# Optimization experiments

Hardware: AMD Instinct MI355X
Metric: run time of the kernel (lower is better)

Reference implementation:

```python
import jax, jax.numpy as jnp
import numpy as np


def setup_inputs() -> dict:
    key = jax.random.key(0)
    ks = jax.random.split(key, 8)
    B, S, H = 2, 2048, 2048
    Hq, Hkv, D = 16, 4, H // 16
    s = 0.02
    return {
        "query": jax.random.normal(ks[0], (B, S, H), jnp.float32),
        "key": jax.random.normal(ks[1], (B, S, H), jnp.float32),
        "value": jax.random.normal(ks[2], (B, S, H), jnp.float32),
        "Wq": jax.random.normal(ks[3], (H, Hq * D), jnp.float32) * s,
        "bq": jnp.zeros((Hq * D,), jnp.float32),
        "Wk": jax.random.normal(ks[4], (H, Hkv * D), jnp.float32) * s,
        "bk": jnp.zeros((Hkv * D,), jnp.float32),
        "Wv": jax.random.normal(ks[5], (H, Hkv * D), jnp.float32) * s,
        "bv": jnp.zeros((Hkv * D,), jnp.float32),
        "Wo": jax.random.normal(ks[6], (H, H), jnp.float32) * s,
        "bo": jnp.zeros((H,), jnp.float32),
    }


def reference(query, key, value, Wq, bq, Wk, bk, Wv, bv, Wo, bo):
    Hq, Hkv = 16, 4
    B, S, H = query.shape
    D = H // Hq
    G = Hq // Hkv  # heads per KV group
    # projections
    q = query @ Wq + bq   # [B,S,Hq*D]
    k = key @ Wk + bk     # [B,S,Hkv*D]
    v = value @ Wv + bv   # [B,S,Hkv*D]
    # [B, Hkv(groups), G(heads per group), S, D] for q; [B, Hkv, S, D] for k,v
    q = q.reshape(B, S, Hkv, G, D).transpose(0, 2, 3, 1, 4)
    k = k.reshape(B, S, Hkv, D).transpose(0, 2, 1, 3)
    v = v.reshape(B, S, Hkv, D).transpose(0, 2, 1, 3)
    # NOTE: original module applies NO 1/sqrt(D) scaling -- kept faithful.
    attn = jnp.einsum('bghqd,bgkd->bghqk', q, k)  # [B,Hkv,G,S,S]
    attn = jax.nn.softmax(attn, axis=-1)
    out = jnp.einsum('bghqk,bgkd->bghqd', attn, v)  # [B,Hkv,G,S,D]
    # permute(0,3,1,2,4) -> [B,S,Hkv,G,D] -> [B,S,H]
    out = out.transpose(0, 3, 1, 2, 4).reshape(B, S, H)
    return out @ Wo + bo
```

## Files before the change

### kernel.cpp

```cpp
#include <hip/hip_runtime.h>
#include <hip/hip_bf16.h>
#include <type_traits>
#include <stdint.h>

typedef short bf16x8 __attribute__((ext_vector_type(8)));
typedef float f32x4 __attribute__((ext_vector_type(4)));

#define GLL16(gp, lp) __builtin_amdgcn_global_load_lds( \
    (const __attribute__((address_space(1))) void*)(gp), \
    (__attribute__((address_space(3))) void*)(lp), 16, 0, 0)

__device__ inline short f2bf(float f) {
    union { float f; uint32_t u; } v;
    v.f = f;
    uint32_t r = (v.u + 0x7FFFu + ((v.u >> 16) & 1u)) >> 16;
    return (short)(uint16_t)r;
}

__device__ inline bf16x8 cvt8(const float4& a, const float4& b) {
    bf16x8 o;
    o[0] = f2bf(a.x); o[1] = f2bf(a.y); o[2] = f2bf(a.z); o[3] = f2bf(a.w);
    o[4] = f2bf(b.x); o[5] = f2bf(b.y); o[6] = f2bf(b.z); o[7] = f2bf(b.w);
    return o;
}

__global__ __launch_bounds__(256) void cvtk(const float* __restrict__ in,
                                            short* __restrict__ out, int n8)
{
    int i = blockIdx.x * blockDim.x + threadIdx.x;
    int stride = gridDim.x * blockDim.x;
    for (; i < n8; i += stride) {
        const float4* p = (const float4*)(in + (size_t)i * 8);
        float4 a = p[0], b = p[1];
        *(bf16x8*)(out + (size_t)i * 8) = cvt8(a, b);
    }
}

__global__ __launch_bounds__(256) void cvt3(
    const float* __restrict__ q, const float* __restrict__ k, const float* __restrict__ v,
    short* __restrict__ Xq, short* __restrict__ Xk, short* __restrict__ Xv)
{
    const float* in; short* out;
    if (blockIdx.y == 0) { in = q; out = Xq; }
    else if (blockIdx.y == 1) { in = k; out = Xk; }
    else { in = v; out = Xv; }
    size_t i = (size_t)blockIdx.x * 256 + threadIdx.x;
    const float4* p = (const float4*)(in + i * 8);
    float4 a = p[0], b = p[1];
    *(bf16x8*)(out + i * 8) = cvt8(a, b);
}

__global__ __launch_bounds__(256) void transW4(
    const float* __restrict__ W0, const float* __restrict__ W1,
    const float* __restrict__ W2, const float* __restrict__ W3,
    short* __restrict__ T0, short* __restrict__ T1,
    short* __restrict__ T2, short* __restrict__ T3)
{
    const int K = 2048;
    const float* W; short* T; int N;
    int z = blockIdx.z;
    if (z == 0)      { W = W0; T = T0; N = 2048; }
    else if (z == 1) { W = W1; T = T1; N = 512; }
    else if (z == 2) { W = W2; T = T2; N = 512; }
    else             { W = W3; T = T3; N = 2048; }
    int n0 = blockIdx.x * 64, k0 = blockIdx.y * 64;
    if (n0 >= N) return;
    __shared__ short Tt[64][65];
    int t = threadIdx.x;
    int kl = t >> 2, nb = (t & 3) * 16;
    const float* wp = W + (size_t)(k0 + kl) * N + n0 + nb;
    #pragma unroll
    for (int j = 0; j < 16; ++j) Tt[nb + j][kl] = f2bf(wp[j]);
    __syncthreads();
    int nl = t >> 2, kb = (t & 3) * 16;
    short* op = T + (size_t)(n0 + nl) * K + k0 + kb;
    #pragma unroll
    for (int j = 0; j < 16; ++j) op[j] = Tt[nl][kb + j];
}

__global__ __launch_bounds__(256) void transV(const short* __restrict__ Vb,
                                              short* __restrict__ Vt)
{
    __shared__ short T[64][65];
    int s0 = blockIdx.x * 64, d0 = blockIdx.y * 64, bg = blockIdx.z;
    int b = bg >> 2, g = bg & 3;
    int t = threadIdx.x;
    int sl = t >> 2, db = (t & 3) * 16;
    const short* vp = Vb + (size_t)(b * 2048 + s0 + sl) * 512 + g * 128 + d0 + db;
    #pragma unroll
    for (int j = 0; j < 16; ++j) T[db + j][sl] = vp[j];
    __syncthreads();
    int dl = t >> 2, sb = (t & 3) * 16;
    short* op = Vt + (size_t)(bg * 128 + d0 + dl) * 2048 + s0 + sb;
    #pragma unroll
    for (int j = 0; j < 16; ++j) op[j] = T[dl][sb + j];
}

template <typename TC>
__device__ __forceinline__ void gemm_core(
    const short* __restrict__ A, const short* __restrict__ BT,
    const float* __restrict__ bias, TC* __restrict__ C,
    int N, int K, int m0, int n0, short* As, short* Bs)
{
    const int t = threadIdx.x, w = t >> 6, lane = t & 63;
    const int lr = lane & 15, lg = lane >> 4;
    const int wm = (w >> 1) * 64, wn = (w & 1) * 64;
    f32x4 acc[4][4] = {};

    const int lrow = lane >> 3;
    const int lcg = (lane & 7) ^ (lrow & 7);
    const int sw = lr & 7;

    const short* abase[2]; const short* bbase[2];
    #pragma unroll
    for (int kc = 0; kc < 2; ++kc) {
        abase[kc] = &As[(wm + lr) * 64 + (((kc * 4 + lg) ^ sw) * 8)];
        bbase[kc] = &Bs[(wn + lr) * 64 + (((kc * 4 + lg) ^ sw) * 8)];
    }
    const short* asrc = A  + (size_t)(m0 + w * 32 + lrow) * K + lcg * 8;
    const short* bsrc = BT + (size_t)(n0 + w * 32 + lrow) * K + lcg * 8;
    short* adst = &As[(w * 32) * 64];
    short* bdst = &Bs[(w * 32) * 64];

    for (int kk = 0; kk < K; kk += 64) {
        __syncthreads();
        #pragma unroll
        for (int i = 0; i < 4; ++i) {
            GLL16(asrc + (size_t)i * 8 * K, adst + i * 512);
            GLL16(bsrc + (size_t)i * 8 * K, bdst + i * 512);
        }
        asrc += 64; bsrc += 64;
        __syncthreads();
        #pragma unroll
        for (int kc = 0; kc < 2; ++kc) {
            bf16x8 af[4], bfr[4];
            #pragma unroll
            for (int i = 0; i < 4; ++i) af[i] = *(const bf16x8*)(abase[kc] + i * 1024);
            #pragma unroll
            for (int j = 0; j < 4; ++j) bfr[j] = *(const bf16x8*)(bbase[kc] + j * 1024);
            #pragma unroll
            for (int i = 0; i < 4; ++i)
                #pragma unroll
                for (int j = 0; j < 4; ++j)
                    acc[i][j] = __builtin_amdgcn_mfma_f32_16x16x32_bf16(af[i], bfr[j], acc[i][j], 0, 0, 0);
        }
    }

    #pragma unroll
    for (int i = 0; i < 4; ++i) {
        #pragma unroll
        for (int j = 0; j < 4; ++j) {
            #pragma unroll
            for (int r = 0; r < 4; ++r) {
                int row = m0 + wm + i * 16 + lg * 4 + r;
                int col = n0 + wn + j * 16 + lr;
                float v = acc[i][j][r] + bias[col];
                if constexpr (std::is_same<TC, short>::value)
                    C[(size_t)row * N + col] = f2bf(v);
                else
                    C[(size_t)row * N + col] = v;
            }
        }
    }
}

template <typename TC>
__global__ __launch_bounds__(256) void gemm_std(
    const short* __restrict__ A, const short* __restrict__ BT,
    const float* __restrict__ bias, TC* __restrict__ C, int N, int K)
{
    __shared__ short As[128 * 64];
    __shared__ short Bs[128 * 64];
    int bid = blockIdx.x;
    int chunk = gridDim.x >> 3;
    int wg = (bid & 7) * chunk + (bid >> 3);
    int m0 = (wg & 31) * 128, n0 = (wg >> 5) * 128;
    gemm_core<TC>(A, BT, bias, C, N, K, m0, n0, As, Bs);
}

__global__ __launch_bounds__(256) void gemm_qkv(
    const short* __restrict__ Xq, const short* __restrict__ Xk, const short* __restrict__ Xv,
    const short* __restrict__ WqT, const short* __restrict__ WkT, const short* __restrict__ WvT,
    const float* __restrict__ bq, const float* __restrict__ bk, const float* __restrict__ bv,
    short* __restrict__ Qb, short* __restrict__ Kb, short* __restrict__ Vb)
{
    __shared__ short As[128 * 64];
    __shared__ short Bs[128 * 64];
    int bid = blockIdx.x;
    int wg = (bid & 7) * 96 + (bid >> 3);
    const short* A; const short* BT; const float* bi; short* C; int N; int l;
    if (wg < 512)      { l = wg;      A = Xq; BT = WqT; bi = bq; C = Qb; N = 2048; }
    else if (wg < 640) { l = wg - 512; A = Xk; BT = WkT; bi = bk; C = Kb; N = 512; }
    else               { l = wg - 640; A = Xv; BT = WvT; bi = bv; C = Vb; N = 512; }
    int m0 = (l & 31) * 128, n0 = (l >> 5) * 128;
    gemm_core<short>(A, BT, bi, C, N, 2048, m0, n0, As, Bs);
}

__global__ __launch_bounds__(256, 4) void attn_kernel(
    const short* __restrict__ Qb, const short* __restrict__ Kb,
    const short* __restrict__ Vt, short* __restrict__ Ob)
{
    const int S = 2048;
    __shared__ short Ks[64 * 128];
    __shared__ short Vs[128 * 64];
    __shared__ short Pl[4][8 * 128];

    const int qt = blockIdx.x, bh = blockIdx.y;
    const int b = bh >> 4, h = bh & 15, g = h >> 2, bg = b * 4 + g;
    const int t = threadIdx.x, w = t >> 6, lane = t & 63;
    const int lr = lane & 15, lg = lane >> 4;
    const int q0 = qt * 64 + w * 16;
    const float C = 1.44269504089f;

    const short* qrow = Qb + ((size_t)(b * S + q0 + lr) * 2048) + h * 128;
    bf16x8 qf[4];
    #pragma unroll
    for (int kc = 0; kc < 4; ++kc)
        qf[kc] = *(const bf16x8*)(qrow + kc * 32 + lg * 8);

    f32x4 ao[8] = {};
    float m_r[4], l_r[4];
    #pragma unroll
    for (int r = 0; r < 4; ++r) { m_r[r] = -1e30f; l_r[r] = 0.0f; }

    const int sw = lr & 7;
    const short* kbase[4];
    #pragma unroll
    for (int kc = 0; kc < 4; ++kc)
        kbase[kc] = &Ks[lr * 128 + (((kc * 4 + lg) ^ sw) * 8)];
    const short* vbase[2];
    #pragma unroll
    for (int kc = 0; kc < 2; ++kc)
        vbase[kc] = &Vs[lr * 64 + (((kc * 4 + lg) ^ sw) * 8)];
    short* Pw = &Pl[w][0];
    short* pwb = Pw + ((lr >> 3) * 128 + lg * 32 + (lr & 7));
    const short* prb = Pw + (lg * 128 + lr * 8);

    const int Lr4 = lane >> 4, Lc4 = lane & 15;
    const int Lr3 = lane >> 3, Lc3 = lane & 7;
    const short* ksrc[4]; const short* vsrc[4];
    #pragma unroll
    for (int i = 0; i < 4; ++i) {
        int kr = w * 16 + i * 4 + Lr4;
        ksrc[i] = Kb + (size_t)(b * S + kr) * 512 + g * 128 + (Lc4 ^ (kr & 7)) * 8;
        int vr = w * 32 + i * 8 + Lr3;
        vsrc[i] = Vt + (size_t)(bg * 128 + vr) * 2048 + (Lc3 ^ (vr & 7)) * 8;
    }
    short* kdst = &Ks[(w * 16) * 128];
    short* vdst = &Vs[(w * 32) * 64];

    for (int kv0 = 0; kv0 < S; kv0 += 64) {
        __syncthreads();
        #pragma unroll
        for (int i = 0; i < 4; ++i) {
            GLL16(ksrc[i], kdst + i * 512);
            GLL16(vsrc[i], vdst + i * 512);
        }
        #pragma unroll
        for (int i = 0; i < 4; ++i) { ksrc[i] += 64 * 512; vsrc[i] += 64; }
        __syncthreads();

        f32x4 sc[4] = {};
        #pragma unroll
        for (int kc = 0; kc < 4; ++kc) {
            #pragma unroll
            for (int f = 0; f < 4; ++f) {
                bf16x8 kfr = *(const bf16x8*)(kbase[kc] + f * 2048);
                sc[f] = __builtin_amdgcn_mfma_f32_16x16x32_bf16(qf[kc], kfr, sc[f], 0, 0, 0);
            }
        }

        float mx[4];
        #pragma unroll
        for (int r = 0; r < 4; ++r) {
            float m = fmaxf(fmaxf(sc[0][r], sc[1][r]), fmaxf(sc[2][r], sc[3][r]));
            m = fmaxf(m, __shfl_xor(m, 1));
            m = fmaxf(m, __shfl_xor(m, 2));
            m = fmaxf(m, __shfl_xor(m, 4));
            m = fmaxf(m, __shfl_xor(m, 8));
            mx[r] = m;
        }
        bool need = (mx[0] > m_r[0]) | (mx[1] > m_r[1]) | (mx[2] > m_r[2]) | (mx[3] > m_r[3]);
        if (__any(need)) {
            float sf[4];
            #pragma unroll
            for (int r = 0; r < 4; ++r) {
                float mnew = fmaxf(m_r[r], mx[r]);
                sf[r] = exp2f((m_r[r] - mnew) * C);
                m_r[r] = mnew;
                l_r[r] *= sf[r];
            }
            #pragma unroll
            for (int d0 = 0; d0 < 8; ++d0)
                #pragma unroll
                for (int r = 0; r < 4; ++r)
                    ao[d0][r] *= sf[r];
        }
        #pragma unroll
        for (int r = 0; r < 4; ++r) {
            float nmc = -m_r[r] * C;
            float p0 = exp2f(fmaf(sc[0][r], C, nmc));
            float p1 = exp2f(fmaf(sc[1][r], C, nmc));
            float p2 = exp2f(fmaf(sc[2][r], C, nmc));
            float p3 = exp2f(fmaf(sc[3][r], C, nmc));
            float rs = (p0 + p1) + (p2 + p3);
            rs += __shfl_xor(rs, 1);
            rs += __shfl_xor(rs, 2);
            rs += __shfl_xor(rs, 4);
            rs += __shfl_xor(rs, 8);
            l_r[r] += rs;
            pwb[0 * 256 + r * 8] = f2bf(p0);
            pwb[1 * 256 + r * 8] = f2bf(p1);
            pwb[2 * 256 + r * 8] = f2bf(p2);
            pwb[3 * 256 + r * 8] = f2bf(p3);
        }

        bf16x8 pf0 = *(const bf16x8*)(prb);
        bf16x8 pf1 = *(const bf16x8*)(prb + 512);
        #pragma unroll
        for (int d0 = 0; d0 < 8; ++d0) {
            bf16x8 v0 = *(const bf16x8*)(vbase[0] + d0 * 1024);
            bf16x8 v1 = *(const bf16x8*)(vbase[1] + d0 * 1024);
            ao[d0] = __builtin_amdgcn_mfma_f32_16x16x32_bf16(pf0, v0, ao[d0], 0, 0, 0);
            ao[d0] = __builtin_amdgcn_mfma_f32_16x16x32_bf16(pf1, v1, ao[d0], 0, 0, 0);
        }
    }

    #pragma unroll
    for (int d0 = 0; d0 < 8; ++d0) {
        #pragma unroll
        for (int r = 0; r < 4; ++r) {
            float v = ao[d0][r] / l_r[r];
            int q = q0 + lg * 4 + r;
            Ob[(size_t)(b * S + q) * 2048 + h * 128 + d0 * 16 + lr] = f2bf(v);
        }
    }
}

extern "C" void kernel_launch(void* const* d_in, const int* in_sizes, int n_in,
                              void* d_out, int out_size, void* d_ws, size_t ws_size,
                              hipStream_t stream)
{
    const float* query = (const float*)d_in[0];
    const float* key   = (const float*)d_in[1];
    const float* value = (const float*)d_in[2];
    const float* Wq    = (const float*)d_in[3];
    const float* bq    = (const float*)d_in[4];
    const float* Wk    = (const float*)d_in[5];
    const float* bk    = (const float*)d_in[6];
    const float* Wv    = (const float*)d_in[7];
    const float* bv    = (const float*)d_in[8];
    const float* Wo    = (const float*)d_in[9];
    const float* bo    = (const float*)d_in[10];
    float* out = (float*)d_out;

    const int BS = 4096;
    char* ws = (char*)d_ws;
    dim3 blk(256);

    if (ws_size >= (size_t)100663296) {
        short* Xq  = (short*)(ws + 0);
        short* Xk  = (short*)(ws + 16777216);
        short* Xv  = (short*)(ws + 33554432);
        short* Qb  = (short*)(ws + 50331648);
        short* Kb  = (short*)(ws + 67108864);
        short* Vb  = (short*)(ws + 71303168);
        short* Vtg = (short*)(ws + 75497472);
        short* WqT = (short*)(ws + 79691776);
        short* WkT = (short*)(ws + 88080384);
        short* WvT = (short*)(ws + 90177536);
        short* WoT = (short*)(ws + 92274688);
        short* Ob  = Xq;

        transW4<<<dim3(32, 32, 4), blk, 0, stream>>>(Wq, Wk, Wv, Wo, WqT, WkT, WvT, WoT);
        cvt3<<<dim3(4096, 3), blk, 0, stream>>>(query, key, value, Xq, Xk, Xv);
        gemm_qkv<<<768, blk, 0, stream>>>(Xq, Xk, Xv, WqT, WkT, WvT, bq, bk, bv, Qb, Kb, Vb);
        transV<<<dim3(32, 2, 8), blk, 0, stream>>>(Vb, Vtg);
        attn_kernel<<<dim3(32, 32), blk, 0, stream>>>(Qb, Kb, Vtg, Ob);
        gemm_std<float><<<512, blk, 0, stream>>>(Ob, WoT, bo, out, 2048, 2048);
    } else {
        short* Qb  = (short*)(ws + 0);
        short* Kb  = (short*)(ws + 16777216);
        short* Vb  = (short*)(ws + 20971520);
        short* Vtg = (short*)(ws + 25165824);
        short* WqT = (short*)(ws + 29360128);
        short* WkT = (short*)(ws + 37748736);
        short* WvT = (short*)(ws + 39845888);
        short* WoT = (short*)(ws + 41943040);
        short* Xbf = (short*)(ws + 50331648);

        transW4<<<dim3(32, 32, 4), blk, 0, stream>>>(Wq, Wk, Wv, Wo, WqT, WkT, WvT, WoT);
        cvtk<<<2048, blk, 0, stream>>>(query, Xbf, BS * 2048 / 8);
        gemm_std<short><<<512, blk, 0, stream>>>(Xbf, WqT, bq, Qb, 2048, 2048);
        cvtk<<<2048, blk, 0, stream>>>(key, Xbf, BS * 2048 / 8);
        gemm_std<short><<<128, blk, 0, stream>>>(Xbf, WkT, bk, Kb, 512, 2048);
        cvtk<<<2048, blk, 0, stream>>>(value, Xbf, BS * 2048 / 8);
        gemm_std<short><<<128, blk, 0, stream>>>(Xbf, WvT, bv, Vb, 512, 2048);
        transV<<<dim3(32, 2, 8), blk, 0, stream>>>(Vb, Vtg);
        attn_kernel<<<dim3(32, 32), blk, 0, stream>>>(Qb, Kb, Vtg, Xbf);
        gemm_std<float><<<512, blk, 0, stream>>>(Xbf, WoT, bo, out, 2048, 2048);
    }
}
```

Baseline: 313.8 us.

## Rewrite attention with 32x32 MFMA, transposed scores, register P and double-buffered K/V

The attention kernel moves from 16x16x32 to 32x32x16 MFMA tiles and computes S^T so each lane owns one query row. Softmax then needs only one cross-half shuffle. P is packed to bf16 in registers and exchanged with lane shuffles instead of going through LDS, K/V tiles are double-buffered so the next tile loads while the current one computes, and block IDs are remapped for locality. Each block now covers 128 query rows and occupancy is halved (launch bounds 2), trading more registers per thread for fewer LDS round-trips and more MFMA reuse of K/V.

```diff
diff --git a/kernel.cpp b/kernel.cpp
--- a/kernel.cpp
+++ b/kernel.cpp
@@ -4,7 +4,9 @@
 #include <stdint.h>
 
 typedef short bf16x8 __attribute__((ext_vector_type(8)));
+typedef short short4v __attribute__((ext_vector_type(4)));
 typedef float f32x4 __attribute__((ext_vector_type(4)));
+typedef float f32x16 __attribute__((ext_vector_type(16)));
 
 #define GLL16(gp, lp) __builtin_amdgcn_global_load_lds( \
     (const __attribute__((address_space(1))) void*)(gp), \
@@ -22,6 +24,31 @@
     o[0] = f2bf(a.x); o[1] = f2bf(a.y); o[2] = f2bf(a.z); o[3] = f2bf(a.w);
     o[4] = f2bf(b.x); o[5] = f2bf(b.y); o[6] = f2bf(b.z); o[7] = f2bf(b.w);
     return o;
+}
+
+__device__ inline uint32_t cvtpk(float lo, float hi) {
+    uint32_t r;
+    asm("v_cvt_pk_bf16_f32 %0, %1, %2" : "=v"(r) : "v"(lo), "v"(hi));
+    return r;
+}
+
+__device__ inline bf16x8 mk8(uint32_t a, uint32_t b, uint32_t c, uint32_t d) {
+    union { uint32_t u[4]; bf16x8 v; } t;
+    t.u[0] = a; t.u[1] = b; t.u[2] = c; t.u[3] = d;
+    return t.v;
+}
+
+__device__ inline void xchg_pf(const uint32_t c[8], bool hib, bf16x8& fA, bf16x8& fB) {
+    uint32_t p0 = (uint32_t)__shfl_xor((int)c[0], 32);
+    uint32_t p1 = (uint32_t)__shfl_xor((int)c[1], 32);
+    uint32_t p2 = (uint32_t)__shfl_xor((int)c[2], 32);
+    uint32_t p3 = (uint32_t)__shfl_xor((int)c[3], 32);
+    fA = mk8(hib ? p2 : c[0], hib ? p3 : c[1], hib ? c[2] : p0, hib ? c[3] : p1);
+    uint32_t p4 = (uint32_t)__shfl_xor((int)c[4], 32);
+    uint32_t p5 = (uint32_t)__shfl_xor((int)c[5], 32);
+    uint32_t p6 = (uint32_t)__shfl_xor((int)c[6], 32);
+    uint32_t p7 = (uint32_t)__shfl_xor((int)c[7], 32);
+    fB = mk8(hib ? p6 : c[4], hib ? p7 : c[5], hib ? c[6] : p4, hib ? c[7] : p5);
 }
 
 __global__ __launch_bounds__(256) void cvtk(const float* __restrict__ in,
@@ -189,150 +216,148 @@
     int bid = blockIdx.x;
     int wg = (bid & 7) * 96 + (bid >> 3);
     const short* A; const short* BT; const float* bi; short* C; int N; int l;
-    if (wg < 512)      { l = wg;      A = Xq; BT = WqT; bi = bq; C = Qb; N = 2048; }
+    if (wg < 512)      { l = wg;       A = Xq; BT = WqT; bi = bq; C = Qb; N = 2048; }
     else if (wg < 640) { l = wg - 512; A = Xk; BT = WkT; bi = bk; C = Kb; N = 512; }
     else               { l = wg - 640; A = Xv; BT = WvT; bi = bv; C = Vb; N = 512; }
     int m0 = (l & 31) * 128, n0 = (l >> 5) * 128;
     gemm_core<short>(A, BT, bi, C, N, 2048, m0, n0, As, Bs);
 }
 
-__global__ __launch_bounds__(256, 4) void attn_kernel(
+__global__ __launch_bounds__(256, 2) void attn_kernel(
     const short* __restrict__ Qb, const short* __restrict__ Kb,
     const short* __restrict__ Vt, short* __restrict__ Ob)
 {
     const int S = 2048;
-    __shared__ short Ks[64 * 128];
-    __shared__ short Vs[128 * 64];
-    __shared__ short Pl[4][8 * 128];
-
-    const int qt = blockIdx.x, bh = blockIdx.y;
+    __shared__ short Ks[2 * 64 * 128];
+    __shared__ short Vs[2 * 128 * 64];
+
+    int bid = blockIdx.x;
+    int wg = (bid & 7) * 64 + (bid >> 3);
+    const int qt = wg & 15, bh = wg >> 4;
     const int b = bh >> 4, h = bh & 15, g = h >> 2, bg = b * 4 + g;
+
     const int t = threadIdx.x, w = t >> 6, lane = t & 63;
-    const int lr = lane & 15, lg = lane >> 4;
-    const int q0 = qt * 64 + w * 16;
+    const int l5 = lane & 31, hi = lane >> 5;
+    const bool hib = hi != 0;
+    const int qg = b * S + qt * 128 + w * 32 + l5;
     const float C = 1.44269504089f;
 
-    const short* qrow = Qb + ((size_t)(b * S + q0 + lr) * 2048) + h * 128;
-    bf16x8 qf[4];
-    #pragma unroll
-    for (int kc = 0; kc < 4; ++kc)
-        qf[kc] = *(const bf16x8*)(qrow + kc * 32 + lg * 8);
-
-    f32x4 ao[8] = {};
-    float m_r[4], l_r[4];
-    #pragma unroll
-    for (int r = 0; r < 4; ++r) { m_r[r] = -1e30f; l_r[r] = 0.0f; }
-
-    const int sw = lr & 7;
-    const short* kbase[4];
-    #pragma unroll
-    for (int kc = 0; kc < 4; ++kc)
-        kbase[kc] = &Ks[lr * 128 + (((kc * 4 + lg) ^ sw) * 8)];
-    const short* vbase[2];
-    #pragma unroll
-    for (int kc = 0; kc < 2; ++kc)
-        vbase[kc] = &Vs[lr * 64 + (((kc * 4 + lg) ^ sw) * 8)];
-    short* Pw = &Pl[w][0];
-    short* pwb = Pw + ((lr >> 3) * 128 + lg * 32 + (lr & 7));
-    const short* prb = Pw + (lg * 128 + lr * 8);
-
-    const int Lr4 = lane >> 4, Lc4 = lane & 15;
-    const int Lr3 = lane >> 3, Lc3 = lane & 7;
+    const short* qrow = Qb + (size_t)qg * 2048 + h * 128 + hi * 8;
+    bf16x8 qf[8];
+    #pragma unroll
+    for (int dm = 0; dm < 8; ++dm)
+        qf[dm] = *(const bf16x8*)(qrow + dm * 16);
+
+    f32x16 o[4] = {};
+    float m = -1e30f, l = 0.0f;
+
+    const int sr4 = lane >> 4, sc4 = lane & 15;
+    const int sr8 = lane >> 3, sc8 = lane & 7;
     const short* ksrc[4]; const short* vsrc[4];
     #pragma unroll
     for (int i = 0; i < 4; ++i) {
-        int kr = w * 16 + i * 4 + Lr4;
-        ksrc[i] = Kb + (size_t)(b * S + kr) * 512 + g * 128 + (Lc4 ^ (kr & 7)) * 8;
-        int vr = w * 32 + i * 8 + Lr3;
-        vsrc[i] = Vt + (size_t)(bg * 128 + vr) * 2048 + (Lc3 ^ (vr & 7)) * 8;
-    }
-    short* kdst = &Ks[(w * 16) * 128];
-    short* vdst = &Vs[(w * 32) * 64];
-
-    for (int kv0 = 0; kv0 < S; kv0 += 64) {
+        int kr = w * 16 + i * 4 + sr4;
+        ksrc[i] = Kb + (size_t)(b * S + kr) * 512 + g * 128 + ((sc4 ^ (kr & 15)) * 8);
+        int d = w * 32 + i * 8 + sr8;
+        vsrc[i] = Vt + (size_t)(bg * 128 + d) * 2048 + ((sc8 ^ (d & 7)) * 8);
+    }
+
+    int kx[8];
+    #pragma unroll
+    for (int dm = 0; dm < 8; ++dm)
+        kx[dm] = (((dm * 2 + hi) ^ (l5 & 15)) * 8);
+    int va[4];
+    #pragma unroll
+    for (int j = 0; j < 4; ++j)
+        va[j] = (((2 * j + hi) ^ (l5 & 7)) * 8);
+
+    #define STAGE(BUF, KVI) do { \
+        short* kd = Ks + (BUF) * 8192 + (w * 16) * 128; \
+        short* vd = Vs + (BUF) * 8192 + (w * 32) * 64; \
+        size_t ko = (size_t)(KVI) * 64 * 512; \
+        int vo = (KVI) * 64; \
+        _Pragma("unroll") \
+        for (int i = 0; i < 4; ++i) { \
+            GLL16(ksrc[i] + ko, kd + i * 512); \
+            GLL16(vsrc[i] + vo, vd + i * 512); \
+        } \
+    } while (0)
+
+    STAGE(0, 0);
+    const int NT = S / 64;
+    for (int ti = 0; ti < NT; ++ti) {
+        int cur = ti & 1;
         __syncthreads();
-        #pragma unroll
-        for (int i = 0; i < 4; ++i) {
-            GLL16(ksrc[i], kdst + i * 512);
-            GLL16(vsrc[i], vdst + i * 512);
-        }
-        #pragma unroll
-        for (int i = 0; i < 4; ++i) { ksrc[i] += 64 * 512; vsrc[i] += 64; }
-        __syncthreads();
-
-        f32x4 sc[4] = {};
-        #pragma unroll
-        for (int kc = 0; kc < 4; ++kc) {
-            #pragma unroll
-            for (int f = 0; f < 4; ++f) {
-                bf16x8 kfr = *(const bf16x8*)(kbase[kc] + f * 2048);
-                sc[f] = __builtin_amdgcn_mfma_f32_16x16x32_bf16(qf[kc], kfr, sc[f], 0, 0, 0);
+        if (ti + 1 < NT) STAGE(cur ^ 1, ti + 1);
+
+        const short* KB = Ks + cur * 8192 + l5 * 128;
+        f32x16 p0 = {}, p1 = {};
+        #pragma unroll
+        for (int dm = 0; dm < 8; ++dm) {
+            bf16x8 k0 = *(const bf16x8*)(KB + kx[dm]);
+            bf16x8 k1 = *(const bf16x8*)(KB + 4096 + kx[dm]);
+            p0 = __builtin_amdgcn_mfma_f32_32x32x16_bf16(k0, qf[dm], p0, 0, 0, 0);
+            p1 = __builtin_amdgcn_mfma_f32_32x32x16_bf16(k1, qf[dm], p1, 0, 0, 0);
+        }
+
+        float mx = -1e30f;
+        #pragma unroll
+        for (int e = 0; e < 16; ++e) mx = fmaxf(mx, fmaxf(p0[e], p1[e]));
+        mx = fmaxf(mx, __shfl_xor(mx, 32));
+        if (__any(mx > m)) {
+            float mn = fmaxf(m, mx);
+            float sf = exp2f((m - mn) * C);
+            m = mn; l *= sf;
+            #pragma unroll
+            for (int dblk = 0; dblk < 4; ++dblk)
+                #pragma unroll
+                for (int e = 0; e < 16; ++e) o[dblk][e] *= sf;
+        }
+        float nmc = -m * C;
+        #pragma unroll
+        for (int e = 0; e < 16; ++e) {
+            p0[e] = exp2f(fmaf(p0[e], C, nmc));
+            p1[e] = exp2f(fmaf(p1[e], C, nmc));
+        }
+        float rs = 0.0f;
+        #pragma unroll
+        for (int e = 0; e < 16; ++e) rs += p0[e] + p1[e];
+        rs += __shfl_xor(rs, 32);
+        l += rs;
+
+        uint32_t c0[8], c1[8];
+        #pragma unroll
+        for (int i = 0; i < 8; ++i) {
+            c0[i] = cvtpk(p0[2 * i], p0[2 * i + 1]);
+            c1[i] = cvtpk(p1[2 * i], p1[2 * i + 1]);
+        }
+        bf16x8 pf[4];
+        xchg_pf(c0, hib, pf[0], pf[1]);
+        xchg_pf(c1, hib, pf[2], pf[3]);
+
+        const short* VB = Vs + cur * 8192 + l5 * 64;
+        #pragma unroll
+        for (int dblk = 0; dblk < 4; ++dblk) {
+            const short* vb = VB + dblk * 2048;
+            #pragma unroll
+            for (int j = 0; j < 4; ++j) {
+                bf16x8 vf = *(const bf16x8*)(vb + va[j]);
+                o[dblk] = __builtin_amdgcn_mfma_f32_32x32x16_bf16(vf, pf[j], o[dblk], 0, 0, 0);
             }
         }
-
-        float mx[4];
-        #pragma unroll
-        for (int r = 0; r < 4; ++r) {
-            float m = fmaxf(fmaxf(sc[0][r], sc[1][r]), fmaxf(sc[2][r], sc[3][r]));
-            m = fmaxf(m, __shfl_xor(m, 1));
-            m = fmaxf(m, __shfl_xor(m, 2));
-            m = fmaxf(m, __shfl_xor(m, 4));
-            m = fmaxf(m, __shfl_xor(m, 8));
-            mx[r] = m;
-        }
-        bool need = (mx[0] > m_r[0]) | (mx[1] > m_r[1]) | (mx[2] > m_r[2]) | (mx[3] > m_r[3]);
-        if (__any(need)) {
-            float sf[4];
-            #pragma unroll
-            for (int r = 0; r < 4; ++r) {
-                float mnew = fmaxf(m_r[r], mx[r]);
-                sf[r] = exp2f((m_r[r] - mnew) * C);
-                m_r[r] = mnew;
-                l_r[r] *= sf[r];
-            }
-            #pragma unroll
-            for (int d0 = 0; d0 < 8; ++d0)
-                #pragma unroll
-                for (int r = 0; r < 4; ++r)
-                    ao[d0][r] *= sf[r];
-        }
-        #pragma unroll
-        for (int r = 0; r < 4; ++r) {
-            float nmc = -m_r[r] * C;
-            float p0 = exp2f(fmaf(sc[0][r], C, nmc));
-            float p1 = exp2f(fmaf(sc[1][r], C, nmc));
-            float p2 = exp2f(fmaf(sc[2][r], C, nmc));
-            float p3 = exp2f(fmaf(sc[3][r], C, nmc));
-            float rs = (p0 + p1) + (p2 + p3);
-            rs += __shfl_xor(rs, 1);
-            rs += __shfl_xor(rs, 2);
-            rs += __shfl_xor(rs, 4);
-            rs += __shfl_xor(rs, 8);
-            l_r[r] += rs;
-            pwb[0 * 256 + r * 8] = f2bf(p0);
-            pwb[1 * 256 + r * 8] = f2bf(p1);
-            pwb[2 * 256 + r * 8] = f2bf(p2);
-            pwb[3 * 256 + r * 8] = f2bf(p3);
-        }
-
-        bf16x8 pf0 = *(const bf16x8*)(prb);
-        bf16x8 pf1 = *(const bf16x8*)(prb + 512);
-        #pragma unroll
-        for (int d0 = 0; d0 < 8; ++d0) {
-            bf16x8 v0 = *(const bf16x8*)(vbase[0] + d0 * 1024);
-            bf16x8 v1 = *(const bf16x8*)(vbase[1] + d0 * 1024);
-            ao[d0] = __builtin_amdgcn_mfma_f32_16x16x32_bf16(pf0, v0, ao[d0], 0, 0, 0);
-            ao[d0] = __builtin_amdgcn_mfma_f32_16x16x32_bf16(pf1, v1, ao[d0], 0, 0, 0);
-        }
-    }
-
-    #pragma unroll
-    for (int d0 = 0; d0 < 8; ++d0) {
-        #pragma unroll
-        for (int r = 0; r < 4; ++r) {
-            float v = ao[d0][r] / l_r[r];
-            int q = q0 + lg * 4 + r;
-            Ob[(size_t)(b * S + q) * 2048 + h * 128 + d0 * 16 + lr] = f2bf(v);
+    }
+    #undef STAGE
+
+    float inv = 1.0f / l;
+    short* op = Ob + (size_t)qg * 2048 + h * 128 + hi * 4;
+    #pragma unroll
+    for (int dblk = 0; dblk < 4; ++dblk) {
+        #pragma unroll
+        for (int mm = 0; mm < 4; ++mm) {
+            short4v s4;
+            #pragma unroll
+            for (int e = 0; e < 4; ++e) s4[e] = f2bf(o[dblk][mm * 4 + e] * inv);
+            *(short4v*)(op + dblk * 32 + mm * 8) = s4;
         }
     }
 }
@@ -376,7 +401,7 @@
         cvt3<<<dim3(4096, 3), blk, 0, stream>>>(query, key, value, Xq, Xk, Xv);
         gemm_qkv<<<768, blk, 0, stream>>>(Xq, Xk, Xv, WqT, WkT, WvT, bq, bk, bv, Qb, Kb, Vb);
         transV<<<dim3(32, 2, 8), blk, 0, stream>>>(Vb, Vtg);
-        attn_kernel<<<dim3(32, 32), blk, 0, stream>>>(Qb, Kb, Vtg, Ob);
+        attn_kernel<<<512, blk, 0, stream>>>(Qb, Kb, Vtg, Ob);
         gemm_std<float><<<512, blk, 0, stream>>>(Ob, WoT, bo, out, 2048, 2048);
     } else {
         short* Qb  = (short*)(ws + 0);
@@ -397,7 +422,7 @@
         cvtk<<<2048, blk, 0, stream>>>(value, Xbf, BS * 2048 / 8);
         gemm_std<short><<<128, blk, 0, stream>>>(Xbf, WvT, bv, Vb, 512, 2048);
         transV<<<dim3(32, 2, 8), blk, 0, stream>>>(Vb, Vtg);
-        attn_kernel<<<dim3(32, 32), blk, 0, stream>>>(Qb, Kb, Vtg, Xbf);
+        attn_kernel<<<512, blk, 0, stream>>>(Qb, Kb, Vtg, Xbf);
         gemm_std<float><<<512, blk, 0, stream>>>(Xbf, WoT, bo, out, 2048, 2048);
     }
 }
```

Result: faster. 266.4 us (-15.1%).
